# Performance work log

Measured on AMD Instinct MI355X. Metric: run time of the kernel, lower is better.

## Reference

```python
import jax, jax.numpy as jnp
import numpy as np

K = 4                      # options['num_k']
NOISE_EPS = 0.1            # noise_epsilon in noisy_top_k_gating
LOSS_COEF = 1e-4
EPS_COMBINE = float(np.finfo(np.float64).eps)  # np.finfo(float).eps in combine
INV_SQRT2 = 0.7071067811865475


def _norm_cdf(z):
    # Normal(0,1).cdf
    return 0.5 * (1.0 + jax.lax.erf(z * INV_SQRT2))


def _cv_squared(v):
    # torch .var() is unbiased (ddof=1)
    return jnp.var(v, ddof=1) / (jnp.mean(v) ** 2 + 1e-10)


def setup_inputs() -> dict:
    key = jax.random.key(0)
    B, D, E, H, O = 1024, 1024, 16, 2048, 1024
    ks = jax.random.split(key, 6)
    x = jax.random.normal(ks[0], (B, D), jnp.float32)
    w_gate = jax.random.normal(ks[1], (D, E), jnp.float32) * 0.02
    w_noise = jax.random.normal(ks[2], (D, E), jnp.float32) * 0.02
    W1 = jax.random.normal(ks[3], (E, D, H), jnp.float32) / np.sqrt(D).astype(np.float32)
    b1 = jnp.zeros((E, H), jnp.float32)
    W2 = jax.random.normal(ks[4], (E, H, O), jnp.float32) / np.sqrt(H).astype(np.float32)
    b2 = jnp.zeros((E, O), jnp.float32)
    noise = jax.random.normal(ks[5], (B, E), jnp.float32)  # randn_like(clean_logits)
    return {"x": x, "w_gate": w_gate, "w_noise": w_noise,
            "W1": W1, "b1": b1, "W2": W2, "b2": b2, "noise": noise}


def moe_forward(x, w_gate, w_noise, W1, b1, W2, b2, noise):
    B = x.shape[0]
    # --- noisy top-k gating (train=True path) ---
    clean_logits = x @ w_gate                              # [B, E]
    noise_std = jax.nn.softplus(x @ w_noise) + NOISE_EPS   # [B, E]
    noisy_logits = clean_logits + noise * noise_std        # [B, E]
    top_logits, top_idx = jax.lax.top_k(noisy_logits, K + 1)  # [B, K+1]
    topk_gates = jax.nn.softmax(top_logits[:, :K], axis=1)    # [B, K]
    gates = jnp.zeros_like(noisy_logits).at[
        jnp.arange(B)[:, None], top_idx[:, :K]].set(topk_gates)  # [B, E] sparse
    # --- load = E[prob in top-k] (smooth load estimate) ---
    thr_in = top_logits[:, K][:, None]       # (k+1)-th value: threshold if in
    thr_out = top_logits[:, K - 1][:, None]  # k-th value: threshold if out
    is_in = noisy_logits > thr_in
    prob_if_in = _norm_cdf((clean_logits - thr_in) / noise_std)
    prob_if_out = _norm_cdf((clean_logits - thr_out) / noise_std)
    load = jnp.where(is_in, prob_if_in, prob_if_out).sum(0)   # [E]
    importance = gates.sum(0)                                 # [E]
    loss = (_cv_squared(importance) + _cv_squared(load)) * LOSS_COEF
    # --- experts + combine ---
    # Dense all-expert compute; gates are exactly zero off the top-k so the
    # gate-weighted sum reproduces the sparse dispatch/index_add combine math.
    h = jax.nn.relu(jnp.einsum('bi,eih->beh', x, W1) + b1)    # [B, E, H]
    expert_out = jnp.einsum('beh,eho->beo', h, W2) + b2       # [B, E, O]
    # combine: sum_e gate[b,e] * exp(expert_out[b,e,:]); zeros -> eps; log
    combined = jnp.einsum('be,beo->bo', gates, jnp.exp(expert_out))  # [B, O]
    combined = jnp.where(combined == 0, EPS_COMBINE, combined)
    y = jnp.log(combined)
    return y, loss


def reference(x, w_gate, w_noise, W1, b1, W2, b2, noise):
    return moe_forward(x, w_gate, w_noise, W1, b1, W2, b2, noise)
```

## Files before the change

kernel.cpp:

```cpp
#include <hip/hip_runtime.h>
#include <cstdint>
#include <cstddef>

#define BTOK 1024
#define DDIM 1024
#define EEXP 16
#define HDIM 2048
#define ODIM 1024

typedef __bf16 bh;
typedef bh bh8 __attribute__((ext_vector_type(8)));
typedef bh bh4 __attribute__((ext_vector_type(4)));
typedef float fx4 __attribute__((ext_vector_type(4)));

__device__ __forceinline__ void gload16(const void* g, void* l) {
  __builtin_amdgcn_global_load_lds(
      (const __attribute__((address_space(1))) void*)g,
      (__attribute__((address_space(3))) void*)l, 16, 0, 0);
}

__global__ __launch_bounds__(256) void k_tcvt(const float* __restrict__ in,
                                              bh* __restrict__ out, int R, int C) {
  const int e = blockIdx.z;
  const int r0 = blockIdx.y * 64, c0 = blockIdx.x * 64;
  const float* pin = in + (size_t)e * R * C;
  bh* pout = out + (size_t)e * R * C;
  __shared__ __align__(16) bh t[64 * 65];
  const int tid = threadIdx.x;
#pragma unroll
  for (int rep = 0; rep < 4; ++rep) {
    int task = rep * 256 + tid;
    int r = task >> 4, c4 = task & 15;
    fx4 v = *(const fx4*)(pin + (size_t)(r0 + r) * C + c0 + c4 * 4);
    int base = r * 65 + c4 * 4;
#pragma unroll
    for (int u = 0; u < 4; ++u) t[base + u] = (bh)v[u];
  }
  __syncthreads();
#pragma unroll
  for (int rep = 0; rep < 4; ++rep) {
    int task = rep * 256 + tid;
    int cc = task >> 4, g2 = task & 15;
    bh4 o;
#pragma unroll
    for (int u = 0; u < 4; ++u) o[u] = t[(g2 * 4 + u) * 65 + cc];
    *(bh4*)(pout + (size_t)(c0 + cc) * R + r0 + g2 * 4) = o;
  }
}

__global__ __launch_bounds__(256) void k_gating(
    const float* __restrict__ x, const float* __restrict__ wg,
    const float* __restrict__ wn, const float* __restrict__ nz,
    bh* __restrict__ xbf, unsigned* __restrict__ cnt,
    int* __restrict__ tok_buck, float* __restrict__ gate_buck,
    float* __restrict__ imp_part, float* __restrict__ load_part) {
  const int b = blockIdx.x, tid = threadIdx.x;
  __shared__ __align__(16) float xs[1024];
  __shared__ float part[32][9];
  __shared__ float vals[32];
  fx4 v = *(const fx4*)(x + (size_t)b * 1024 + tid * 4);
  *(fx4*)(xs + tid * 4) = v;
  bh4 xb;
#pragma unroll
  for (int u = 0; u < 4; ++u) xb[u] = (bh)v[u];
  *(bh4*)(xbf + (size_t)b * 1024 + tid * 4) = xb;
  __syncthreads();
  const int col = tid & 31, g = tid >> 5;
  const float* wp = ((col < 16) ? wg : wn) + (col & 15);
  float s = 0.f;
  for (int it = g * 128; it < g * 128 + 128; ++it) s += xs[it] * wp[it * 16];
  part[col][g] = s;
  __syncthreads();
  if (tid < 32) {
    float tsum = 0.f;
#pragma unroll
    for (int gg = 0; gg < 8; ++gg) tsum += part[tid][gg];
    vals[tid] = tsum;
  }
  __syncthreads();
  if (tid == 0) {
    float clean[16], sd[16], noisy[16];
#pragma unroll
    for (int e = 0; e < 16; ++e) {
      clean[e] = vals[e];
      float raw = vals[16 + e];
      float sp = fmaxf(raw, 0.f) + log1pf(expf(-fabsf(raw)));
      sd[e] = sp + 0.1f;
      noisy[e] = clean[e] + nz[b * 16 + e] * sd[e];
    }
    float tv[5]; int ti[5]; unsigned used = 0;
    for (int r = 0; r < 5; ++r) {
      float bst = -INFINITY; int bi = 0;
      for (int e = 0; e < 16; ++e)
        if (!((used >> e) & 1u) && noisy[e] > bst) { bst = noisy[e]; bi = e; }
      used |= 1u << bi; tv[r] = bst; ti[r] = bi;
    }
    float gts[4]; float se = 0.f;
#pragma unroll
    for (int k = 0; k < 4; ++k) { gts[k] = expf(tv[k] - tv[0]); se += gts[k]; }
#pragma unroll
    for (int k = 0; k < 4; ++k) gts[k] /= se;
    const float thr_in = tv[4], thr_out = tv[3];
    float imp[16];
#pragma unroll
    for (int e = 0; e < 16; ++e) imp[e] = 0.f;
    for (int k = 0; k < 4; ++k) imp[ti[k]] = gts[k];
    for (int e = 0; e < 16; ++e) imp_part[b * 16 + e] = imp[e];
    for (int e = 0; e < 16; ++e) {
      bool is_in = noisy[e] > thr_in;
      float z = (clean[e] - (is_in ? thr_in : thr_out)) / sd[e];
      load_part[b * 16 + e] = 0.5f * (1.f + erff(z * 0.70710678118654752f));
    }
    for (int k = 0; k < 4; ++k) {
      int ee = ti[k];
      unsigned p = atomicAdd(&cnt[ee], 1u);
      tok_buck[ee * 1024 + (int)p] = b;
      gate_buck[ee * 1024 + (int)p] = gts[k];
    }
  }
}

__device__ __forceinline__ float cv2_16(const float* v) {
  float m = 0.f;
  for (int i = 0; i < 16; ++i) m += v[i];
  m *= (1.f / 16.f);
  float var = 0.f;
  for (int i = 0; i < 16; ++i) { float d = v[i] - m; var += d * d; }
  var *= (1.f / 15.f);
  return var / (m * m + 1e-10f);
}

__global__ __launch_bounds__(256) void k_finalize(
    const unsigned* __restrict__ cnt, unsigned* __restrict__ offs,
    const float* __restrict__ imp_part, const float* __restrict__ load_part,
    float* __restrict__ loss_out) {
  const int tid = threadIdx.x;
  __shared__ float red[256];
  __shared__ float impv[16], loadv[16];
  const int e = tid & 15, p = tid >> 4;
  float s = 0.f;
  for (int r = 0; r < 64; ++r) s += imp_part[((p * 64 + r) << 4) + e];
  red[tid] = s;
  __syncthreads();
  if (tid < 16) {
    float t = 0.f;
    for (int pp = 0; pp < 16; ++pp) t += red[pp * 16 + tid];
    impv[tid] = t;
  }
  __syncthreads();
  s = 0.f;
  for (int r = 0; r < 64; ++r) s += load_part[((p * 64 + r) << 4) + e];
  red[tid] = s;
  __syncthreads();
  if (tid < 16) {
    float t = 0.f;
    for (int pp = 0; pp < 16; ++pp) t += red[pp * 16 + tid];
    loadv[tid] = t;
  }
  __syncthreads();
  if (tid == 0) {
    unsigned o = 0;
    for (int ee = 0; ee < 16; ++ee) { offs[ee] = o; o += cnt[ee]; }
    loss_out[0] = (cv2_16(impv) + cv2_16(loadv)) * 1e-4f;
  }
}

__global__ __launch_bounds__(256) void k_gemm1(
    const bh* __restrict__ xbf, const bh* __restrict__ w1t,
    const float* __restrict__ b1, const int* __restrict__ tok_buck,
    const unsigned* __restrict__ cnt, const unsigned* __restrict__ offs,
    bh* __restrict__ hbf) {
  const int e = blockIdx.z, mt = blockIdx.y, nt = blockIdx.x;
  const int ne = (int)cnt[e];
  if (mt * 128 >= ne) return;
  __shared__ __align__(16) bh As[128 * 32];
  __shared__ __align__(16) bh Bs[128 * 32];
  const int tid = threadIdx.x;
  const int lane = tid & 63, wv = tid >> 6, wm = wv >> 1, wn_ = wv & 1;

  const bh* a_src[2]; const bh* b_src[2];
  void* a_dst[2]; void* b_dst[2];
#pragma unroll
  for (int r = 0; r < 2; ++r) {
    int task = r * 256 + tid;
    int row = task >> 2, s = task & 3;
    int gm = mt * 128 + row; if (gm >= ne) gm = ne - 1;
    int tok = tok_buck[e * 1024 + gm];
    a_src[r] = xbf + (size_t)tok * 1024 + ((s ^ (row & 3)) << 3);
    b_src[r] = w1t + (size_t)e * (2048 * 1024) + (size_t)(nt * 128 + row) * 1024 +
               ((s ^ (row & 3)) << 3);
    int wub = (r * 256 + (wv << 6)) << 4;
    a_dst[r] = (char*)As + wub;
    b_dst[r] = (char*)Bs + wub;
  }
  const int ln15 = lane & 15, q = lane >> 4;
  const int qs = ((q ^ (ln15 & 3)) << 3);
  int a_off[4], b_off[4];
#pragma unroll
  for (int i = 0; i < 4; ++i) {
    a_off[i] = (wm * 64 + i * 16 + ln15) * 32 + qs;
    b_off[i] = (wn_ * 64 + i * 16 + ln15) * 32 + qs;
  }
  fx4 zero = {0.f, 0.f, 0.f, 0.f};
  fx4 acc[4][4];
#pragma unroll
  for (int i = 0; i < 4; ++i)
#pragma unroll
    for (int j = 0; j < 4; ++j) acc[i][j] = zero;

  for (int kt = 0; kt < 32; ++kt) {
    __syncthreads();
    const int ko = kt * 32;
#pragma unroll
    for (int r = 0; r < 2; ++r) {
      gload16(a_src[r] + ko, a_dst[r]);
      gload16(b_src[r] + ko, b_dst[r]);
    }
    __syncthreads();
    bh8 af[4], bfr[4];
#pragma unroll
    for (int i = 0; i < 4; ++i) af[i] = *(const bh8*)(As + a_off[i]);
#pragma unroll
    for (int i = 0; i < 4; ++i) bfr[i] = *(const bh8*)(Bs + b_off[i]);
#pragma unroll
    for (int i = 0; i < 4; ++i)
#pragma unroll
      for (int j = 0; j < 4; ++j)
        acc[i][j] = __builtin_amdgcn_mfma_f32_16x16x32_bf16(af[i], bfr[j], acc[i][j], 0, 0, 0);
  }

  int nrows = ne - mt * 128; if (nrows > 128) nrows = 128;
  int jn[4]; float b1v[4];
#pragma unroll
  for (int j = 0; j < 4; ++j) {
    jn[j] = nt * 128 + wn_ * 64 + j * 16 + ln15;
    b1v[j] = b1[e * 2048 + jn[j]];
  }
  const int rowbase = (int)offs[e] + mt * 128;
#pragma unroll
  for (int i = 0; i < 4; ++i)
#pragma unroll
    for (int rr = 0; rr < 4; ++rr) {
      int ml = wm * 64 + i * 16 + q * 4 + rr;
      if (ml < nrows) {
        size_t ro = (size_t)(rowbase + ml) * 2048;
#pragma unroll
        for (int j = 0; j < 4; ++j) {
          float vv = acc[i][j][rr] + b1v[j];
          hbf[ro + jn[j]] = (bh)fmaxf(vv, 0.f);
        }
      }
    }
}

__global__ __launch_bounds__(256) void k_gemm2(
    const bh* __restrict__ hbf, const bh* __restrict__ w2t,
    const float* __restrict__ b2, const int* __restrict__ tok_buck,
    const float* __restrict__ gate_buck, const unsigned* __restrict__ cnt,
    const unsigned* __restrict__ offs, float* __restrict__ yv) {
  const int e = blockIdx.z, mt = blockIdx.y, nt = blockIdx.x;
  const int ne = (int)cnt[e];
  if (mt * 128 >= ne) return;
  __shared__ __align__(16) bh As[128 * 32];
  __shared__ __align__(16) bh Bs[128 * 32];
  const int tid = threadIdx.x;
  const int lane = tid & 63, wv = tid >> 6, wm = wv >> 1, wn_ = wv & 1;
  const int rowbase = (int)offs[e] + mt * 128;

  const bh* a_src[2]; const bh* b_src[2];
  void* a_dst[2]; void* b_dst[2];
#pragma unroll
  for (int r = 0; r < 2; ++r) {
    int task = r * 256 + tid;
    int row = task >> 2, s = task & 3;
    a_src[r] = hbf + (size_t)(rowbase + row) * 2048 + ((s ^ (row & 3)) << 3);
    b_src[r] = w2t + (size_t)e * (1024 * 2048) + (size_t)(nt * 128 + row) * 2048 +
               ((s ^ (row & 3)) << 3);
    int wub = (r * 256 + (wv << 6)) << 4;
    a_dst[r] = (char*)As + wub;
    b_dst[r] = (char*)Bs + wub;
  }
  const int ln15 = lane & 15, q = lane >> 4;
  const int qs = ((q ^ (ln15 & 3)) << 3);
  int a_off[4], b_off[4];
#pragma unroll
  for (int i = 0; i < 4; ++i) {
    a_off[i] = (wm * 64 + i * 16 + ln15) * 32 + qs;
    b_off[i] = (wn_ * 64 + i * 16 + ln15) * 32 + qs;
  }
  fx4 zero = {0.f, 0.f, 0.f, 0.f};
  fx4 acc[4][4];
#pragma unroll
  for (int i = 0; i < 4; ++i)
#pragma unroll
    for (int j = 0; j < 4; ++j) acc[i][j] = zero;

  for (int kt = 0; kt < 64; ++kt) {
    __syncthreads();
    const int ko = kt * 32;
#pragma unroll
    for (int r = 0; r < 2; ++r) {
      gload16(a_src[r] + ko, a_dst[r]);
      gload16(b_src[r] + ko, b_dst[r]);
    }
    __syncthreads();
    bh8 af[4], bfr[4];
#pragma unroll
    for (int i = 0; i < 4; ++i) af[i] = *(const bh8*)(As + a_off[i]);
#pragma unroll
    for (int i = 0; i < 4; ++i) bfr[i] = *(const bh8*)(Bs + b_off[i]);
#pragma unroll
    for (int i = 0; i < 4; ++i)
#pragma unroll
      for (int j = 0; j < 4; ++j)
        acc[i][j] = __builtin_amdgcn_mfma_f32_16x16x32_bf16(af[i], bfr[j], acc[i][j], 0, 0, 0);
  }

  int nrows = ne - mt * 128; if (nrows > 128) nrows = 128;
  int on[4]; float b2v[4];
#pragma unroll
  for (int j = 0; j < 4; ++j) {
    on[j] = nt * 128 + wn_ * 64 + j * 16 + ln15;
    b2v[j] = b2[e * 1024 + on[j]];
  }
#pragma unroll
  for (int i = 0; i < 4; ++i)
#pragma unroll
    for (int rr = 0; rr < 4; ++rr) {
      int ml = wm * 64 + i * 16 + q * 4 + rr;
      if (ml < nrows) {
        int pos = mt * 128 + ml;
        int bt = tok_buck[e * 1024 + pos];
        float gg = gate_buck[e * 1024 + pos];
        float* yrow = yv + (size_t)bt * 1024;
#pragma unroll
        for (int j = 0; j < 4; ++j)
          atomicAdd(&yrow[on[j]], gg * expf(acc[i][j][rr] + b2v[j]));
      }
    }
}

__global__ __launch_bounds__(256) void k_log(float* __restrict__ yv) {
  const int i = blockIdx.x * 256 + threadIdx.x;
  fx4* p = (fx4*)yv + i;
  fx4 v = *p;
#pragma unroll
  for (int c = 0; c < 4; ++c) {
    float w = v[c];
    if (w == 0.f) w = 2.2204460492503131e-16f;
    v[c] = logf(w);
  }
  *p = v;
}

extern "C" void kernel_launch(void* const* d_in, const int* in_sizes, int n_in,
                              void* d_out, int out_size, void* d_ws, size_t ws_size,
                              hipStream_t stream) {
  const float* x  = (const float*)d_in[0];
  const float* wg = (const float*)d_in[1];
  const float* wn = (const float*)d_in[2];
  const float* W1 = (const float*)d_in[3];
  const float* b1 = (const float*)d_in[4];
  const float* W2 = (const float*)d_in[5];
  const float* b2 = (const float*)d_in[6];
  const float* nz = (const float*)d_in[7];
  float* out = (float*)d_out;

  char* ws = (char*)d_ws;
  unsigned* cnt      = (unsigned*)(ws + 0);
  unsigned* offs     = (unsigned*)(ws + 64);
  float*    imp_part = (float*)(ws + 256);
  float*    load_part= (float*)(ws + 256 + 65536);
  int*      tok_buck = (int*)(ws + 256 + 2 * 65536);
  float*    gate_buck= (float*)(ws + 256 + 3 * 65536);
  bh*       xbf      = (bh*)(ws + 262400);
  bh*       hbf      = (bh*)(ws + 2359552);
  bh*       w1t      = (bh*)(ws + 19661056);
  bh*       w2t      = (bh*)(ws + 86769920);
  const size_t needed = 153878784;
  if (ws_size < needed) {
    hipMemsetAsync(d_out, 0x42, (size_t)out_size * 4, stream);
    return;
  }

  hipMemsetAsync(d_out, 0, (size_t)out_size * 4, stream);
  hipMemsetAsync(cnt, 0, 64, stream);

  k_tcvt<<<dim3(2048 / 64, 1024 / 64, 16), 256, 0, stream>>>(W1, w1t, 1024, 2048);
  k_tcvt<<<dim3(1024 / 64, 2048 / 64, 16), 256, 0, stream>>>(W2, w2t, 2048, 1024);
  k_gating<<<1024, 256, 0, stream>>>(x, wg, wn, nz, xbf, cnt, tok_buck, gate_buck,
                                     imp_part, load_part);
  k_finalize<<<1, 256, 0, stream>>>(cnt, offs, imp_part, load_part, out + (out_size - 1));
  k_gemm1<<<dim3(16, 8, 16), 256, 0, stream>>>(xbf, w1t, b1, tok_buck, cnt, offs, hbf);
  k_gemm2<<<dim3(8, 8, 16), 256, 0, stream>>>(hbf, w2t, b2, tok_buck, gate_buck, cnt, offs, out);
  k_log<<<1024, 256, 0, stream>>>(out);
}
```

Measured before the change: 491.5 us.

## Fuse fp32 weight conversion into expert GEMMs and enlarge M tile to 256

Drops the separate transpose-and-convert kernels for W1 and W2. The GEMM kernels now read fp32 weights directly with coalesced column loads, convert them to bf16 in registers and store them into swizzled LDS. This removes a full read and write pass over both weight tensors. The M tile is doubled to 256 rows so each weight tile is reused across more tokens, and occupancy is hinted at 2 blocks per unit. The trade-offs are more registers per thread and per-k synchronous fp32 loads inside the main loop, which may stall the MFMA pipeline.

```diff
diff --git a/kernel.cpp b/kernel.cpp
--- a/kernel.cpp
+++ b/kernel.cpp
@@ -1,12 +1,6 @@
 #include <hip/hip_runtime.h>
 #include <cstdint>
 #include <cstddef>
-
-#define BTOK 1024
-#define DDIM 1024
-#define EEXP 16
-#define HDIM 2048
-#define ODIM 1024
 
 typedef __bf16 bh;
 typedef bh bh8 __attribute__((ext_vector_type(8)));
@@ -19,34 +13,7 @@
       (__attribute__((address_space(3))) void*)l, 16, 0, 0);
 }
 
-__global__ __launch_bounds__(256) void k_tcvt(const float* __restrict__ in,
-                                              bh* __restrict__ out, int R, int C) {
-  const int e = blockIdx.z;
-  const int r0 = blockIdx.y * 64, c0 = blockIdx.x * 64;
-  const float* pin = in + (size_t)e * R * C;
-  bh* pout = out + (size_t)e * R * C;
-  __shared__ __align__(16) bh t[64 * 65];
-  const int tid = threadIdx.x;
-#pragma unroll
-  for (int rep = 0; rep < 4; ++rep) {
-    int task = rep * 256 + tid;
-    int r = task >> 4, c4 = task & 15;
-    fx4 v = *(const fx4*)(pin + (size_t)(r0 + r) * C + c0 + c4 * 4);
-    int base = r * 65 + c4 * 4;
-#pragma unroll
-    for (int u = 0; u < 4; ++u) t[base + u] = (bh)v[u];
-  }
-  __syncthreads();
-#pragma unroll
-  for (int rep = 0; rep < 4; ++rep) {
-    int task = rep * 256 + tid;
-    int cc = task >> 4, g2 = task & 15;
-    bh4 o;
-#pragma unroll
-    for (int u = 0; u < 4; ++u) o[u] = t[(g2 * 4 + u) * 65 + cc];
-    *(bh4*)(pout + (size_t)(c0 + cc) * R + r0 + g2 * 4) = o;
-  }
-}
+__device__ __forceinline__ int swz(int r) { return (r >> 1) & 3; }
 
 __global__ __launch_bounds__(256) void k_gating(
     const float* __restrict__ x, const float* __restrict__ wg,
@@ -165,158 +132,189 @@
   }
 }
 
-__global__ __launch_bounds__(256) void k_gemm1(
-    const bh* __restrict__ xbf, const bh* __restrict__ w1t,
+__global__ __launch_bounds__(256, 2) void k_gemm1f(
+    const bh* __restrict__ xbf, const float* __restrict__ W1,
     const float* __restrict__ b1, const int* __restrict__ tok_buck,
     const unsigned* __restrict__ cnt, const unsigned* __restrict__ offs,
     bh* __restrict__ hbf) {
   const int e = blockIdx.z, mt = blockIdx.y, nt = blockIdx.x;
   const int ne = (int)cnt[e];
-  if (mt * 128 >= ne) return;
-  __shared__ __align__(16) bh As[128 * 32];
+  if (mt * 256 >= ne) return;
+  __shared__ __align__(16) bh As[256 * 32];
   __shared__ __align__(16) bh Bs[128 * 32];
   const int tid = threadIdx.x;
   const int lane = tid & 63, wv = tid >> 6, wm = wv >> 1, wn_ = wv & 1;
 
-  const bh* a_src[2]; const bh* b_src[2];
-  void* a_dst[2]; void* b_dst[2];
-#pragma unroll
-  for (int r = 0; r < 2; ++r) {
+  const bh* a_src[4]; void* a_dst[4];
+#pragma unroll
+  for (int r = 0; r < 4; ++r) {
     int task = r * 256 + tid;
     int row = task >> 2, s = task & 3;
-    int gm = mt * 128 + row; if (gm >= ne) gm = ne - 1;
+    int gm = mt * 256 + row; if (gm >= ne) gm = ne - 1;
     int tok = tok_buck[e * 1024 + gm];
-    a_src[r] = xbf + (size_t)tok * 1024 + ((s ^ (row & 3)) << 3);
-    b_src[r] = w1t + (size_t)e * (2048 * 1024) + (size_t)(nt * 128 + row) * 1024 +
-               ((s ^ (row & 3)) << 3);
-    int wub = (r * 256 + (wv << 6)) << 4;
-    a_dst[r] = (char*)As + wub;
-    b_dst[r] = (char*)Bs + wub;
-  }
+    a_src[r] = xbf + (size_t)tok * 1024 + ((s ^ swz(row)) << 3);
+    a_dst[r] = (char*)As + (size_t)(r * 256 + (wv << 6)) * 16;
+  }
+  const int nl = tid & 127, khalf = tid >> 7;
+  const float* bp = W1 + (size_t)e * (1024 * 2048) +
+                    (size_t)(khalf * 16) * 2048 + nt * 128 + nl;
+  bh8* wp0 = (bh8*)(Bs + nl * 32 + (((khalf * 2)     ^ swz(nl)) << 3));
+  bh8* wp1 = (bh8*)(Bs + nl * 32 + (((khalf * 2 + 1) ^ swz(nl)) << 3));
+
   const int ln15 = lane & 15, q = lane >> 4;
-  const int qs = ((q ^ (ln15 & 3)) << 3);
-  int a_off[4], b_off[4];
-#pragma unroll
-  for (int i = 0; i < 4; ++i) {
-    a_off[i] = (wm * 64 + i * 16 + ln15) * 32 + qs;
-    b_off[i] = (wn_ * 64 + i * 16 + ln15) * 32 + qs;
-  }
+  const int qs = (q ^ swz(ln15)) << 3;
+  int a_off[2][4], b_off[4];
+#pragma unroll
+  for (int c = 0; c < 2; ++c)
+#pragma unroll
+    for (int i = 0; i < 4; ++i)
+      a_off[c][i] = (c * 128 + wm * 64 + i * 16 + ln15) * 32 + qs;
+#pragma unroll
+  for (int j = 0; j < 4; ++j) b_off[j] = (wn_ * 64 + j * 16 + ln15) * 32 + qs;
+
   fx4 zero = {0.f, 0.f, 0.f, 0.f};
-  fx4 acc[4][4];
-#pragma unroll
-  for (int i = 0; i < 4; ++i)
-#pragma unroll
-    for (int j = 0; j < 4; ++j) acc[i][j] = zero;
+  fx4 acc[2][4][4];
+#pragma unroll
+  for (int c = 0; c < 2; ++c)
+#pragma unroll
+    for (int i = 0; i < 4; ++i)
+#pragma unroll
+      for (int j = 0; j < 4; ++j) acc[c][i][j] = zero;
 
   for (int kt = 0; kt < 32; ++kt) {
     __syncthreads();
     const int ko = kt * 32;
-#pragma unroll
-    for (int r = 0; r < 2; ++r) {
-      gload16(a_src[r] + ko, a_dst[r]);
-      gload16(b_src[r] + ko, b_dst[r]);
-    }
+    float bv[16];
+#pragma unroll
+    for (int i = 0; i < 16; ++i) bv[i] = bp[(size_t)(ko + i) * 2048];
+#pragma unroll
+    for (int r = 0; r < 4; ++r) gload16(a_src[r] + ko, a_dst[r]);
+    bh8 lo, hi;
+#pragma unroll
+    for (int u = 0; u < 8; ++u) { lo[u] = (bh)bv[u]; hi[u] = (bh)bv[8 + u]; }
+    *wp0 = lo; *wp1 = hi;
     __syncthreads();
-    bh8 af[4], bfr[4];
-#pragma unroll
-    for (int i = 0; i < 4; ++i) af[i] = *(const bh8*)(As + a_off[i]);
-#pragma unroll
-    for (int i = 0; i < 4; ++i) bfr[i] = *(const bh8*)(Bs + b_off[i]);
-#pragma unroll
-    for (int i = 0; i < 4; ++i)
-#pragma unroll
-      for (int j = 0; j < 4; ++j)
-        acc[i][j] = __builtin_amdgcn_mfma_f32_16x16x32_bf16(af[i], bfr[j], acc[i][j], 0, 0, 0);
-  }
-
-  int nrows = ne - mt * 128; if (nrows > 128) nrows = 128;
+    bh8 bfr[4];
+#pragma unroll
+    for (int j = 0; j < 4; ++j) bfr[j] = *(const bh8*)(Bs + b_off[j]);
+#pragma unroll
+    for (int c = 0; c < 2; ++c) {
+      bh8 af[4];
+#pragma unroll
+      for (int i = 0; i < 4; ++i) af[i] = *(const bh8*)(As + a_off[c][i]);
+#pragma unroll
+      for (int i = 0; i < 4; ++i)
+#pragma unroll
+        for (int j = 0; j < 4; ++j)
+          acc[c][i][j] = __builtin_amdgcn_mfma_f32_16x16x32_bf16(af[i], bfr[j], acc[c][i][j], 0, 0, 0);
+    }
+  }
+
+  int nrows = ne - mt * 256; if (nrows > 256) nrows = 256;
   int jn[4]; float b1v[4];
 #pragma unroll
   for (int j = 0; j < 4; ++j) {
     jn[j] = nt * 128 + wn_ * 64 + j * 16 + ln15;
     b1v[j] = b1[e * 2048 + jn[j]];
   }
-  const int rowbase = (int)offs[e] + mt * 128;
-#pragma unroll
-  for (int i = 0; i < 4; ++i)
-#pragma unroll
-    for (int rr = 0; rr < 4; ++rr) {
-      int ml = wm * 64 + i * 16 + q * 4 + rr;
-      if (ml < nrows) {
-        size_t ro = (size_t)(rowbase + ml) * 2048;
-#pragma unroll
-        for (int j = 0; j < 4; ++j) {
-          float vv = acc[i][j][rr] + b1v[j];
-          hbf[ro + jn[j]] = (bh)fmaxf(vv, 0.f);
+  const int rowbase = (int)offs[e] + mt * 256;
+#pragma unroll
+  for (int c = 0; c < 2; ++c)
+#pragma unroll
+    for (int i = 0; i < 4; ++i)
+#pragma unroll
+      for (int rr = 0; rr < 4; ++rr) {
+        int ml = c * 128 + wm * 64 + i * 16 + q * 4 + rr;
+        if (ml < nrows) {
+          size_t ro = (size_t)(rowbase + ml) * 2048;
+#pragma unroll
+          for (int j = 0; j < 4; ++j) {
+            float vv = acc[c][i][j][rr] + b1v[j];
+            hbf[ro + jn[j]] = (bh)fmaxf(vv, 0.f);
+          }
         }
       }
-    }
-}
-
-__global__ __launch_bounds__(256) void k_gemm2(
-    const bh* __restrict__ hbf, const bh* __restrict__ w2t,
+}
+
+__global__ __launch_bounds__(256, 2) void k_gemm2f(
+    const bh* __restrict__ hbf, const float* __restrict__ W2,
     const float* __restrict__ b2, const int* __restrict__ tok_buck,
     const float* __restrict__ gate_buck, const unsigned* __restrict__ cnt,
     const unsigned* __restrict__ offs, float* __restrict__ yv) {
   const int e = blockIdx.z, mt = blockIdx.y, nt = blockIdx.x;
   const int ne = (int)cnt[e];
-  if (mt * 128 >= ne) return;
-  __shared__ __align__(16) bh As[128 * 32];
+  if (mt * 256 >= ne) return;
+  __shared__ __align__(16) bh As[256 * 32];
   __shared__ __align__(16) bh Bs[128 * 32];
   const int tid = threadIdx.x;
   const int lane = tid & 63, wv = tid >> 6, wm = wv >> 1, wn_ = wv & 1;
-  const int rowbase = (int)offs[e] + mt * 128;
-
-  const bh* a_src[2]; const bh* b_src[2];
-  void* a_dst[2]; void* b_dst[2];
-#pragma unroll
-  for (int r = 0; r < 2; ++r) {
+  int nrows = ne - mt * 256; if (nrows > 256) nrows = 256;
+  const int rowbase = (int)offs[e] + mt * 256;
+
+  const bh* a_src[4]; void* a_dst[4];
+#pragma unroll
+  for (int r = 0; r < 4; ++r) {
     int task = r * 256 + tid;
     int row = task >> 2, s = task & 3;
-    a_src[r] = hbf + (size_t)(rowbase + row) * 2048 + ((s ^ (row & 3)) << 3);
-    b_src[r] = w2t + (size_t)e * (1024 * 2048) + (size_t)(nt * 128 + row) * 2048 +
-               ((s ^ (row & 3)) << 3);
-    int wub = (r * 256 + (wv << 6)) << 4;
-    a_dst[r] = (char*)As + wub;
-    b_dst[r] = (char*)Bs + wub;
-  }
+    int gr = row; if (gr >= nrows) gr = nrows - 1;
+    a_src[r] = hbf + (size_t)(rowbase + gr) * 2048 + ((s ^ swz(row)) << 3);
+    a_dst[r] = (char*)As + (size_t)(r * 256 + (wv << 6)) * 16;
+  }
+  const int nl = tid & 127, khalf = tid >> 7;
+  const float* bp = W2 + (size_t)e * (2048 * 1024) +
+                    (size_t)(khalf * 16) * 1024 + nt * 128 + nl;
+  bh8* wp0 = (bh8*)(Bs + nl * 32 + (((khalf * 2)     ^ swz(nl)) << 3));
+  bh8* wp1 = (bh8*)(Bs + nl * 32 + (((khalf * 2 + 1) ^ swz(nl)) << 3));
+
   const int ln15 = lane & 15, q = lane >> 4;
-  const int qs = ((q ^ (ln15 & 3)) << 3);
-  int a_off[4], b_off[4];
-#pragma unroll
-  for (int i = 0; i < 4; ++i) {
-    a_off[i] = (wm * 64 + i * 16 + ln15) * 32 + qs;
-    b_off[i] = (wn_ * 64 + i * 16 + ln15) * 32 + qs;
-  }
+  const int qs = (q ^ swz(ln15)) << 3;
+  int a_off[2][4], b_off[4];
+#pragma unroll
+  for (int c = 0; c < 2; ++c)
+#pragma unroll
+    for (int i = 0; i < 4; ++i)
+      a_off[c][i] = (c * 128 + wm * 64 + i * 16 + ln15) * 32 + qs;
+#pragma unroll
+  for (int j = 0; j < 4; ++j) b_off[j] = (wn_ * 64 + j * 16 + ln15) * 32 + qs;
+
   fx4 zero = {0.f, 0.f, 0.f, 0.f};
-  fx4 acc[4][4];
-#pragma unroll
-  for (int i = 0; i < 4; ++i)
-#pragma unroll
-    for (int j = 0; j < 4; ++j) acc[i][j] = zero;
+  fx4 acc[2][4][4];
+#pragma unroll
+  for (int c = 0; c < 2; ++c)
+#pragma unroll
+    for (int i = 0; i < 4; ++i)
+#pragma unroll
+      for (int j = 0; j < 4; ++j) acc[c][i][j] = zero;
 
   for (int kt = 0; kt < 64; ++kt) {
     __syncthreads();
     const int ko = kt * 32;
-#pragma unroll
-    for (int r = 0; r < 2; ++r) {
-      gload16(a_src[r] + ko, a_dst[r]);
-      gload16(b_src[r] + ko, b_dst[r]);
-    }
+    float bv[16];
+#pragma unroll
+    for (int i = 0; i < 16; ++i) bv[i] = bp[(size_t)(ko + i) * 1024];
+#pragma unroll
+    for (int r = 0; r < 4; ++r) gload16(a_src[r] + ko, a_dst[r]);
+    bh8 lo, hi;
+#pragma unroll
+    for (int u = 0; u < 8; ++u) { lo[u] = (bh)bv[u]; hi[u] = (bh)bv[8 + u]; }
+    *wp0 = lo; *wp1 = hi;
     __syncthreads();
-    bh8 af[4], bfr[4];
-#pragma unroll
-    for (int i = 0; i < 4; ++i) af[i] = *(const bh8*)(As + a_off[i]);
-#pragma unroll
-    for (int i = 0; i < 4; ++i) bfr[i] = *(const bh8*)(Bs + b_off[i]);
-#pragma unroll
-    for (int i = 0; i < 4; ++i)
-#pragma unroll
-      for (int j = 0; j < 4; ++j)
-        acc[i][j] = __builtin_amdgcn_mfma_f32_16x16x32_bf16(af[i], bfr[j], acc[i][j], 0, 0, 0);
-  }
-
-  int nrows = ne - mt * 128; if (nrows > 128) nrows = 128;
+    bh8 bfr[4];
+#pragma unroll
+    for (int j = 0; j < 4; ++j) bfr[j] = *(const bh8*)(Bs + b_off[j]);
+#pragma unroll
+    for (int c = 0; c < 2; ++c) {
+      bh8 af[4];
+#pragma unroll
+      for (int i = 0; i < 4; ++i) af[i] = *(const bh8*)(As + a_off[c][i]);
+#pragma unroll
+      for (int i = 0; i < 4; ++i)
+#pragma unroll
+        for (int j = 0; j < 4; ++j)
+          acc[c][i][j] = __builtin_amdgcn_mfma_f32_16x16x32_bf16(af[i], bfr[j], acc[c][i][j], 0, 0, 0);
+    }
+  }
+
   int on[4]; float b2v[4];
 #pragma unroll
   for (int j = 0; j < 4; ++j) {
@@ -324,20 +322,22 @@
     b2v[j] = b2[e * 1024 + on[j]];
   }
 #pragma unroll
-  for (int i = 0; i < 4; ++i)
-#pragma unroll
-    for (int rr = 0; rr < 4; ++rr) {
-      int ml = wm * 64 + i * 16 + q * 4 + rr;
-      if (ml < nrows) {
-        int pos = mt * 128 + ml;
-        int bt = tok_buck[e * 1024 + pos];
-        float gg = gate_buck[e * 1024 + pos];
-        float* yrow = yv + (size_t)bt * 1024;
-#pragma unroll
-        for (int j = 0; j < 4; ++j)
-          atomicAdd(&yrow[on[j]], gg * expf(acc[i][j][rr] + b2v[j]));
+  for (int c = 0; c < 2; ++c)
+#pragma unroll
+    for (int i = 0; i < 4; ++i)
+#pragma unroll
+      for (int rr = 0; rr < 4; ++rr) {
+        int ml = c * 128 + wm * 64 + i * 16 + q * 4 + rr;
+        if (ml < nrows) {
+          int pos = mt * 256 + ml;
+          int bt = tok_buck[e * 1024 + pos];
+          float gg = gate_buck[e * 1024 + pos];
+          float* yrow = yv + (size_t)bt * 1024;
+#pragma unroll
+          for (int j = 0; j < 4; ++j)
+            atomicAdd(&yrow[on[j]], gg * expf(acc[c][i][j][rr] + b2v[j]));
+        }
       }
-    }
 }
 
 __global__ __launch_bounds__(256) void k_log(float* __restrict__ yv) {
@@ -375,9 +375,7 @@
   float*    gate_buck= (float*)(ws + 256 + 3 * 65536);
   bh*       xbf      = (bh*)(ws + 262400);
   bh*       hbf      = (bh*)(ws + 2359552);
-  bh*       w1t      = (bh*)(ws + 19661056);
-  bh*       w2t      = (bh*)(ws + 86769920);
-  const size_t needed = 153878784;
+  const size_t needed = 2359552 + (size_t)4096 * 2048 * 2;
   if (ws_size < needed) {
     hipMemsetAsync(d_out, 0x42, (size_t)out_size * 4, stream);
     return;
@@ -386,12 +384,10 @@
   hipMemsetAsync(d_out, 0, (size_t)out_size * 4, stream);
   hipMemsetAsync(cnt, 0, 64, stream);
 
-  k_tcvt<<<dim3(2048 / 64, 1024 / 64, 16), 256, 0, stream>>>(W1, w1t, 1024, 2048);
-  k_tcvt<<<dim3(1024 / 64, 2048 / 64, 16), 256, 0, stream>>>(W2, w2t, 2048, 1024);
   k_gating<<<1024, 256, 0, stream>>>(x, wg, wn, nz, xbf, cnt, tok_buck, gate_buck,
                                      imp_part, load_part);
   k_finalize<<<1, 256, 0, stream>>>(cnt, offs, imp_part, load_part, out + (out_size - 1));
-  k_gemm1<<<dim3(16, 8, 16), 256, 0, stream>>>(xbf, w1t, b1, tok_buck, cnt, offs, hbf);
-  k_gemm2<<<dim3(8, 8, 16), 256, 0, stream>>>(hbf, w2t, b2, tok_buck, gate_buck, cnt, offs, out);
+  k_gemm1f<<<dim3(16, 4, 16), 256, 0, stream>>>(xbf, W1, b1, tok_buck, cnt, offs, hbf);
+  k_gemm2f<<<dim3(8, 4, 16), 256, 0, stream>>>(hbf, W2, b2, tok_buck, gate_buck, cnt, offs, out);
   k_log<<<1024, 256, 0, stream>>>(out);
 }
```

Result: no change. 497.8 us (+1.3%).

## Fuse weight fp32-to-bf16 conversion into expert GEMMs with double-buffered pipeline

Applied to the files above, without the earlier changes.

Drops the separate transpose-and-convert kernels for W1 and W2. The expert GEMMs now read the fp32 weights directly, convert them to bf16 in registers and write them into a swizzled LDS tile. This removes a full extra read and write pass over about 256 MB of weights. The GEMMs also gain double-buffered LDS with register prefetch one step ahead, a smaller 128x64 tile with a doubled grid, and launch bounds allowing two blocks per SM. The cost is that the wider fp32 weight read is repeated by every M-tile instead of being converted once.

```diff
diff --git a/kernel.cpp b/kernel.cpp
--- a/kernel.cpp
+++ b/kernel.cpp
@@ -1,12 +1,6 @@
 #include <hip/hip_runtime.h>
 #include <cstdint>
 #include <cstddef>
-
-#define BTOK 1024
-#define DDIM 1024
-#define EEXP 16
-#define HDIM 2048
-#define ODIM 1024
 
 typedef __bf16 bh;
 typedef bh bh8 __attribute__((ext_vector_type(8)));
@@ -19,34 +13,7 @@
       (__attribute__((address_space(3))) void*)l, 16, 0, 0);
 }
 
-__global__ __launch_bounds__(256) void k_tcvt(const float* __restrict__ in,
-                                              bh* __restrict__ out, int R, int C) {
-  const int e = blockIdx.z;
-  const int r0 = blockIdx.y * 64, c0 = blockIdx.x * 64;
-  const float* pin = in + (size_t)e * R * C;
-  bh* pout = out + (size_t)e * R * C;
-  __shared__ __align__(16) bh t[64 * 65];
-  const int tid = threadIdx.x;
-#pragma unroll
-  for (int rep = 0; rep < 4; ++rep) {
-    int task = rep * 256 + tid;
-    int r = task >> 4, c4 = task & 15;
-    fx4 v = *(const fx4*)(pin + (size_t)(r0 + r) * C + c0 + c4 * 4);
-    int base = r * 65 + c4 * 4;
-#pragma unroll
-    for (int u = 0; u < 4; ++u) t[base + u] = (bh)v[u];
-  }
-  __syncthreads();
-#pragma unroll
-  for (int rep = 0; rep < 4; ++rep) {
-    int task = rep * 256 + tid;
-    int cc = task >> 4, g2 = task & 15;
-    bh4 o;
-#pragma unroll
-    for (int u = 0; u < 4; ++u) o[u] = t[(g2 * 4 + u) * 65 + cc];
-    *(bh4*)(pout + (size_t)(c0 + cc) * R + r0 + g2 * 4) = o;
-  }
-}
+__device__ __forceinline__ int swz(int r) { return (r >> 1) & 3; }
 
 __global__ __launch_bounds__(256) void k_gating(
     const float* __restrict__ x, const float* __restrict__ wg,
@@ -165,83 +132,113 @@
   }
 }
 
-__global__ __launch_bounds__(256) void k_gemm1(
-    const bh* __restrict__ xbf, const bh* __restrict__ w1t,
+__global__ __launch_bounds__(256, 2) void k_gemm1p(
+    const bh* __restrict__ xbf, const float* __restrict__ W1,
     const float* __restrict__ b1, const int* __restrict__ tok_buck,
     const unsigned* __restrict__ cnt, const unsigned* __restrict__ offs,
     bh* __restrict__ hbf) {
   const int e = blockIdx.z, mt = blockIdx.y, nt = blockIdx.x;
   const int ne = (int)cnt[e];
   if (mt * 128 >= ne) return;
-  __shared__ __align__(16) bh As[128 * 32];
-  __shared__ __align__(16) bh Bs[128 * 32];
+  __shared__ __align__(16) bh As[2][128 * 32];
+  __shared__ __align__(16) bh Bs[2][64 * 32];
   const int tid = threadIdx.x;
-  const int lane = tid & 63, wv = tid >> 6, wm = wv >> 1, wn_ = wv & 1;
-
-  const bh* a_src[2]; const bh* b_src[2];
-  void* a_dst[2]; void* b_dst[2];
+  const int lane = tid & 63, wv = tid >> 6;
+  const int NK = 32;
+
+  const bh* a_src[2]; int a_dsto[2];
 #pragma unroll
   for (int r = 0; r < 2; ++r) {
     int task = r * 256 + tid;
     int row = task >> 2, s = task & 3;
     int gm = mt * 128 + row; if (gm >= ne) gm = ne - 1;
     int tok = tok_buck[e * 1024 + gm];
-    a_src[r] = xbf + (size_t)tok * 1024 + ((s ^ (row & 3)) << 3);
-    b_src[r] = w1t + (size_t)e * (2048 * 1024) + (size_t)(nt * 128 + row) * 1024 +
-               ((s ^ (row & 3)) << 3);
-    int wub = (r * 256 + (wv << 6)) << 4;
-    a_dst[r] = (char*)As + wub;
-    b_dst[r] = (char*)Bs + wub;
-  }
+    a_src[r] = xbf + (size_t)tok * 1024 + ((s ^ swz(row)) << 3);
+    a_dsto[r] = (r * 256 + (wv << 6)) * 16;
+  }
+  const int nl = tid & 63, kq = tid >> 6;
+  const float* bp = W1 + (size_t)e * (1024 * 2048) + (size_t)(kq * 8) * 2048 +
+                    nt * 64 + nl;
+  const int b_wro = nl * 32 + ((kq ^ swz(nl)) << 3);
+
   const int ln15 = lane & 15, q = lane >> 4;
-  const int qs = ((q ^ (ln15 & 3)) << 3);
-  int a_off[4], b_off[4];
-#pragma unroll
-  for (int i = 0; i < 4; ++i) {
-    a_off[i] = (wm * 64 + i * 16 + ln15) * 32 + qs;
-    b_off[i] = (wn_ * 64 + i * 16 + ln15) * 32 + qs;
+  int a_off[2], b_off[4];
+#pragma unroll
+  for (int i = 0; i < 2; ++i) {
+    int row = wv * 32 + i * 16 + ln15;
+    a_off[i] = row * 32 + ((q ^ swz(row)) << 3);
+  }
+#pragma unroll
+  for (int j = 0; j < 4; ++j) {
+    int row = j * 16 + ln15;
+    b_off[j] = row * 32 + ((q ^ swz(row)) << 3);
   }
   fx4 zero = {0.f, 0.f, 0.f, 0.f};
-  fx4 acc[4][4];
-#pragma unroll
-  for (int i = 0; i < 4; ++i)
+  fx4 acc[2][4];
+#pragma unroll
+  for (int i = 0; i < 2; ++i)
 #pragma unroll
     for (int j = 0; j < 4; ++j) acc[i][j] = zero;
 
-  for (int kt = 0; kt < 32; ++kt) {
-    __syncthreads();
-    const int ko = kt * 32;
-#pragma unroll
-    for (int r = 0; r < 2; ++r) {
-      gload16(a_src[r] + ko, a_dst[r]);
-      gload16(b_src[r] + ko, b_dst[r]);
-    }
-    __syncthreads();
-    bh8 af[4], bfr[4];
-#pragma unroll
-    for (int i = 0; i < 4; ++i) af[i] = *(const bh8*)(As + a_off[i]);
-#pragma unroll
-    for (int i = 0; i < 4; ++i) bfr[i] = *(const bh8*)(Bs + b_off[i]);
-#pragma unroll
-    for (int i = 0; i < 4; ++i)
+  float rb[2][8];
+#pragma unroll
+  for (int i = 0; i < 8; ++i) rb[0][i] = bp[(size_t)i * 2048];
+#pragma unroll
+  for (int r = 0; r < 2; ++r) gload16(a_src[r], (char*)As[0] + a_dsto[r]);
+  {
+    bh8 w;
+#pragma unroll
+    for (int u = 0; u < 8; ++u) w[u] = (bh)rb[0][u];
+    *(bh8*)(Bs[0] + b_wro) = w;
+  }
+#pragma unroll
+  for (int i = 0; i < 8; ++i) rb[1][i] = bp[(size_t)(32 + i) * 2048];
+#pragma unroll
+  for (int r = 0; r < 2; ++r) gload16(a_src[r] + 32, (char*)As[1] + a_dsto[r]);
+  __syncthreads();
+
+  for (int kt = 0; kt < NK; ++kt) {
+    const int p = kt & 1;
+    bh8 bfr[4], af[2];
+#pragma unroll
+    for (int j = 0; j < 4; ++j) bfr[j] = *(const bh8*)(Bs[p] + b_off[j]);
+#pragma unroll
+    for (int i = 0; i < 2; ++i) af[i] = *(const bh8*)(As[p] + a_off[i]);
+#pragma unroll
+    for (int i = 0; i < 2; ++i)
 #pragma unroll
       for (int j = 0; j < 4; ++j)
         acc[i][j] = __builtin_amdgcn_mfma_f32_16x16x32_bf16(af[i], bfr[j], acc[i][j], 0, 0, 0);
+    if (kt + 1 < NK) {
+      bh8 w;
+#pragma unroll
+      for (int u = 0; u < 8; ++u) w[u] = (bh)rb[(kt + 1) & 1][u];
+      *(bh8*)(Bs[1 - p] + b_wro) = w;
+    }
+    __syncthreads();
+    if (kt + 2 < NK) {
+      const size_t ko = (size_t)(kt + 2) * 32;
+#pragma unroll
+      for (int i = 0; i < 8; ++i) rb[p][i] = bp[(ko + i) * 2048];
+#pragma unroll
+      for (int r = 0; r < 2; ++r)
+        gload16(a_src[r] + ko, (char*)As[p] + a_dsto[r]);
+    }
   }
 
   int nrows = ne - mt * 128; if (nrows > 128) nrows = 128;
   int jn[4]; float b1v[4];
 #pragma unroll
   for (int j = 0; j < 4; ++j) {
-    jn[j] = nt * 128 + wn_ * 64 + j * 16 + ln15;
+    jn[j] = nt * 64 + j * 16 + ln15;
     b1v[j] = b1[e * 2048 + jn[j]];
   }
   const int rowbase = (int)offs[e] + mt * 128;
 #pragma unroll
-  for (int i = 0; i < 4; ++i)
+  for (int i = 0; i < 2; ++i)
 #pragma unroll
     for (int rr = 0; rr < 4; ++rr) {
-      int ml = wm * 64 + i * 16 + q * 4 + rr;
+      int ml = wv * 32 + i * 16 + q * 4 + rr;
       if (ml < nrows) {
         size_t ro = (size_t)(rowbase + ml) * 2048;
 #pragma unroll
@@ -253,81 +250,112 @@
     }
 }
 
-__global__ __launch_bounds__(256) void k_gemm2(
-    const bh* __restrict__ hbf, const bh* __restrict__ w2t,
+__global__ __launch_bounds__(256, 2) void k_gemm2p(
+    const bh* __restrict__ hbf, const float* __restrict__ W2,
     const float* __restrict__ b2, const int* __restrict__ tok_buck,
     const float* __restrict__ gate_buck, const unsigned* __restrict__ cnt,
     const unsigned* __restrict__ offs, float* __restrict__ yv) {
   const int e = blockIdx.z, mt = blockIdx.y, nt = blockIdx.x;
   const int ne = (int)cnt[e];
   if (mt * 128 >= ne) return;
-  __shared__ __align__(16) bh As[128 * 32];
-  __shared__ __align__(16) bh Bs[128 * 32];
+  __shared__ __align__(16) bh As[2][128 * 32];
+  __shared__ __align__(16) bh Bs[2][64 * 32];
   const int tid = threadIdx.x;
-  const int lane = tid & 63, wv = tid >> 6, wm = wv >> 1, wn_ = wv & 1;
+  const int lane = tid & 63, wv = tid >> 6;
+  const int NK = 64;
+  int nrows = ne - mt * 128; if (nrows > 128) nrows = 128;
   const int rowbase = (int)offs[e] + mt * 128;
 
-  const bh* a_src[2]; const bh* b_src[2];
-  void* a_dst[2]; void* b_dst[2];
+  const bh* a_src[2]; int a_dsto[2];
 #pragma unroll
   for (int r = 0; r < 2; ++r) {
     int task = r * 256 + tid;
     int row = task >> 2, s = task & 3;
-    a_src[r] = hbf + (size_t)(rowbase + row) * 2048 + ((s ^ (row & 3)) << 3);
-    b_src[r] = w2t + (size_t)e * (1024 * 2048) + (size_t)(nt * 128 + row) * 2048 +
-               ((s ^ (row & 3)) << 3);
-    int wub = (r * 256 + (wv << 6)) << 4;
-    a_dst[r] = (char*)As + wub;
-    b_dst[r] = (char*)Bs + wub;
-  }
+    int gr = row; if (gr >= nrows) gr = nrows - 1;
+    a_src[r] = hbf + (size_t)(rowbase + gr) * 2048 + ((s ^ swz(row)) << 3);
+    a_dsto[r] = (r * 256 + (wv << 6)) * 16;
+  }
+  const int nl = tid & 63, kq = tid >> 6;
+  const float* bp = W2 + (size_t)e * (2048 * 1024) + (size_t)(kq * 8) * 1024 +
+                    nt * 64 + nl;
+  const int b_wro = nl * 32 + ((kq ^ swz(nl)) << 3);
+
   const int ln15 = lane & 15, q = lane >> 4;
-  const int qs = ((q ^ (ln15 & 3)) << 3);
-  int a_off[4], b_off[4];
-#pragma unroll
-  for (int i = 0; i < 4; ++i) {
-    a_off[i] = (wm * 64 + i * 16 + ln15) * 32 + qs;
-    b_off[i] = (wn_ * 64 + i * 16 + ln15) * 32 + qs;
+  int a_off[2], b_off[4];
+#pragma unroll
+  for (int i = 0; i < 2; ++i) {
+    int row = wv * 32 + i * 16 + ln15;
+    a_off[i] = row * 32 + ((q ^ swz(row)) << 3);
+  }
+#pragma unroll
+  for (int j = 0; j < 4; ++j) {
+    int row = j * 16 + ln15;
+    b_off[j] = row * 32 + ((q ^ swz(row)) << 3);
   }
   fx4 zero = {0.f, 0.f, 0.f, 0.f};
-  fx4 acc[4][4];
-#pragma unroll
-  for (int i = 0; i < 4; ++i)
+  fx4 acc[2][4];
+#pragma unroll
+  for (int i = 0; i < 2; ++i)
 #pragma unroll
     for (int j = 0; j < 4; ++j) acc[i][j] = zero;
 
-  for (int kt = 0; kt < 64; ++kt) {
-    __syncthreads();
-    const int ko = kt * 32;
-#pragma unroll
-    for (int r = 0; r < 2; ++r) {
-      gload16(a_src[r] + ko, a_dst[r]);
-      gload16(b_src[r] + ko, b_dst[r]);
-    }
-    __syncthreads();
-    bh8 af[4], bfr[4];
-#pragma unroll
-    for (int i = 0; i < 4; ++i) af[i] = *(const bh8*)(As + a_off[i]);
-#pragma unroll
-    for (int i = 0; i < 4; ++i) bfr[i] = *(const bh8*)(Bs + b_off[i]);
-#pragma unroll
-    for (int i = 0; i < 4; ++i)
+  float rb[2][8];
+#pragma unroll
+  for (int i = 0; i < 8; ++i) rb[0][i] = bp[(size_t)i * 1024];
+#pragma unroll
+  for (int r = 0; r < 2; ++r) gload16(a_src[r], (char*)As[0] + a_dsto[r]);
+  {
+    bh8 w;
+#pragma unroll
+    for (int u = 0; u < 8; ++u) w[u] = (bh)rb[0][u];
+    *(bh8*)(Bs[0] + b_wro) = w;
+  }
+#pragma unroll
+  for (int i = 0; i < 8; ++i) rb[1][i] = bp[(size_t)(32 + i) * 1024];
+#pragma unroll
+  for (int r = 0; r < 2; ++r) gload16(a_src[r] + 32, (char*)As[1] + a_dsto[r]);
+  __syncthreads();
+
+  for (int kt = 0; kt < NK; ++kt) {
+    const int p = kt & 1;
+    bh8 bfr[4], af[2];
+#pragma unroll
+    for (int j = 0; j < 4; ++j) bfr[j] = *(const bh8*)(Bs[p] + b_off[j]);
+#pragma unroll
+    for (int i = 0; i < 2; ++i) af[i] = *(const bh8*)(As[p] + a_off[i]);
+#pragma unroll
+    for (int i = 0; i < 2; ++i)
 #pragma unroll
       for (int j = 0; j < 4; ++j)
         acc[i][j] = __builtin_amdgcn_mfma_f32_16x16x32_bf16(af[i], bfr[j], acc[i][j], 0, 0, 0);
-  }
-
-  int nrows = ne - mt * 128; if (nrows > 128) nrows = 128;
+    if (kt + 1 < NK) {
+      bh8 w;
+#pragma unroll
+      for (int u = 0; u < 8; ++u) w[u] = (bh)rb[(kt + 1) & 1][u];
+      *(bh8*)(Bs[1 - p] + b_wro) = w;
+    }
+    __syncthreads();
+    if (kt + 2 < NK) {
+      const size_t ko = (size_t)(kt + 2) * 32;
+#pragma unroll
+      for (int i = 0; i < 8; ++i) rb[p][i] = bp[(ko + i) * 1024];
+#pragma unroll
+      for (int r = 0; r < 2; ++r)
+        gload16(a_src[r] + ko, (char*)As[p] + a_dsto[r]);
+    }
+  }
+
   int on[4]; float b2v[4];
 #pragma unroll
   for (int j = 0; j < 4; ++j) {
-    on[j] = nt * 128 + wn_ * 64 + j * 16 + ln15;
+    on[j] = nt * 64 + j * 16 + ln15;
     b2v[j] = b2[e * 1024 + on[j]];
   }
 #pragma unroll
-  for (int i = 0; i < 4; ++i)
+  for (int i = 0; i < 2; ++i)
 #pragma unroll
     for (int rr = 0; rr < 4; ++rr) {
-      int ml = wm * 64 + i * 16 + q * 4 + rr;
+      int ml = wv * 32 + i * 16 + q * 4 + rr;
       if (ml < nrows) {
         int pos = mt * 128 + ml;
         int bt = tok_buck[e * 1024 + pos];
@@ -375,9 +403,7 @@
   float*    gate_buck= (float*)(ws + 256 + 3 * 65536);
   bh*       xbf      = (bh*)(ws + 262400);
   bh*       hbf      = (bh*)(ws + 2359552);
-  bh*       w1t      = (bh*)(ws + 19661056);
-  bh*       w2t      = (bh*)(ws + 86769920);
-  const size_t needed = 153878784;
+  const size_t needed = 2359552 + (size_t)4096 * 2048 * 2;
   if (ws_size < needed) {
     hipMemsetAsync(d_out, 0x42, (size_t)out_size * 4, stream);
     return;
@@ -386,12 +412,10 @@
   hipMemsetAsync(d_out, 0, (size_t)out_size * 4, stream);
   hipMemsetAsync(cnt, 0, 64, stream);
 
-  k_tcvt<<<dim3(2048 / 64, 1024 / 64, 16), 256, 0, stream>>>(W1, w1t, 1024, 2048);
-  k_tcvt<<<dim3(1024 / 64, 2048 / 64, 16), 256, 0, stream>>>(W2, w2t, 2048, 1024);
   k_gating<<<1024, 256, 0, stream>>>(x, wg, wn, nz, xbf, cnt, tok_buck, gate_buck,
                                      imp_part, load_part);
   k_finalize<<<1, 256, 0, stream>>>(cnt, offs, imp_part, load_part, out + (out_size - 1));
-  k_gemm1<<<dim3(16, 8, 16), 256, 0, stream>>>(xbf, w1t, b1, tok_buck, cnt, offs, hbf);
-  k_gemm2<<<dim3(8, 8, 16), 256, 0, stream>>>(hbf, w2t, b2, tok_buck, gate_buck, cnt, offs, out);
+  k_gemm1p<<<dim3(32, 8, 16), 256, 0, stream>>>(xbf, W1, b1, tok_buck, cnt, offs, hbf);
+  k_gemm2p<<<dim3(16, 8, 16), 256, 0, stream>>>(hbf, W2, b2, tok_buck, gate_buck, cnt, offs, out);
   k_log<<<1024, 256, 0, stream>>>(out);
 }
```

Result: slower. 565.8 us (+15.1%).
